# Optimization experiments

Measured on AMD Instinct MI355X. Metric: run time of the kernel, lower is better.

The kernel has to match this reference:

```python
import jax, jax.numpy as jnp
import numpy as np

N = 8192
F_IN = 128
F_OUT = 64
ALPHA = 0.2
NEG_INF = -9.0e15  # matches -9000000000000000.0 in the torch source


def setup_inputs() -> dict:
    key = jax.random.key(0)
    k1, k2, k3, k4 = jax.random.split(key, 4)
    h = jax.random.normal(k1, (N, F_IN), dtype=jnp.float32)
    adj = jax.random.randint(k2, (N, N), 0, 2).astype(jnp.int32)
    W = jax.random.normal(k3, (F_IN, F_OUT), dtype=jnp.float32) * 0.05
    a = jax.random.normal(k4, (2 * F_OUT,), dtype=jnp.float32) * 0.05
    return {"h": h, "adj": adj, "W": W, "a": a}


def reference(h, adj, W, a):
    # Wh: [N, F_OUT]
    Wh = h @ W
    # a([Wh_i ; Wh_j]) == Wh_i @ a1 + Wh_j @ a2 -> avoid O(N^2*2F) concat
    a1, a2 = a[:F_OUT], a[F_OUT:]
    s_src = Wh @ a1  # [N] contribution of row node i
    s_dst = Wh @ a2  # [N] contribution of col node j
    e = jax.nn.leaky_relu(s_src[:, None] + s_dst[None, :], negative_slope=ALPHA)  # [N, N]
    e = jnp.where(adj > 0, e, NEG_INF)
    attention = jax.nn.softmax(e, axis=1)  # [N, N]
    h_prime = attention @ Wh  # [N, F_OUT]
    return jax.nn.elu(h_prime)
```

## Files before the change

kernel.cpp:

```cpp
#include <hip/hip_runtime.h>
#include <hip/hip_bf16.h>

#define N 8192
#define FIN 128
#define FOUT 64
#define CSPLIT 4
#define CHUNK (N / CSPLIT)
#define M 32
#define TILE 64
#define NT (CHUNK / TILE)
#define LOG2E 1.44269504f

typedef __attribute__((ext_vector_type(4))) float f32x4;
typedef __attribute__((ext_vector_type(4))) int i32x4;
typedef __attribute__((ext_vector_type(8))) short bf16x8;

#define GLOAD_LDS16(gp, lp)                                                    \
    __builtin_amdgcn_global_load_lds(                                          \
        (const __attribute__((address_space(1))) void*)(gp),                   \
        (__attribute__((address_space(3))) void*)(lp), 16, 0, 0)

__global__ __launch_bounds__(256) void wh_kernel(
    const float* __restrict__ h, const float* __restrict__ W,
    const float* __restrict__ a,
    __hip_bfloat16* __restrict__ whT, float* __restrict__ s_src,
    float* __restrict__ s_dst) {
    __shared__ float Wl[FIN * FOUT];
    const int w = threadIdx.x >> 6;
    const int lane = threadIdx.x & 63;
#pragma unroll
    for (int q = 0; q < 8; ++q) {
        const int i = w * 8 + q;
        GLOAD_LDS16(W + i * 256 + lane * 4, &Wl[i * 256]);
    }
    asm volatile("s_waitcnt vmcnt(0)" ::: "memory");
    __syncthreads();

    const int row = blockIdx.x * 4 + w;
    const float* hr = h + (size_t)row * FIN;
    float acc = 0.f;
#pragma unroll
    for (int k0 = 0; k0 < FIN; k0 += 4) {
        f32x4 hv = *(const f32x4*)(hr + k0);
        acc += hv[0] * Wl[(k0 + 0) * FOUT + lane];
        acc += hv[1] * Wl[(k0 + 1) * FOUT + lane];
        acc += hv[2] * Wl[(k0 + 2) * FOUT + lane];
        acc += hv[3] * Wl[(k0 + 3) * FOUT + lane];
    }
    whT[(size_t)lane * N + row] = __float2bfloat16(acc);
    float s1 = acc * a[lane];
    float s2 = acc * a[FOUT + lane];
#pragma unroll
    for (int mm = 32; mm >= 1; mm >>= 1) {
        s1 += __shfl_xor(s1, mm, 64);
        s2 += __shfl_xor(s2, mm, 64);
    }
    if (lane == 0) { s_src[row] = s1 * LOG2E; s_dst[row] = s2 * LOG2E; }
}

__global__ __launch_bounds__(256, 4) void gat_partial(
    const int* __restrict__ adj, const __hip_bfloat16* __restrict__ whT,
    const float* __restrict__ s_src, const float* __restrict__ s_dst,
    float* __restrict__ numP, float* __restrict__ denP) {
    union SMem {
        struct {
            int adjb[2][M][TILE];
            short whb[2][FOUT][TILE];
            float sdl[CHUNK];
        } s;
        struct { float pC[2][M][FOUT]; float pD[2][M]; } e;
    };
    __shared__ SMem sm;

    const int tid = threadIdx.x;
    const int w = tid >> 6, lane = tid & 63;
    const int m = lane & 15, kg = lane >> 4;
    const int wr = w >> 1, wc = w & 1;
    const int rg = blockIdx.x >> 2;
    const int c = blockIdx.x & 3;
    const int ibase = rg * M;
    const int cb = c * CHUNK;
    const int aRow = wr * 16 + m;
    const float ssrc = s_src[ibase + aRow];
    const int sidx = w * 2;

    f32x4 acc[4] = {{0,0,0,0},{0,0,0,0},{0,0,0,0},{0,0,0,0}};
    f32x4 acc4 = {0,0,0,0};
    const short oneb = (m == 0) ? (short)0x3F80 : (short)0;
    const bf16x8 bones = {oneb, oneb, oneb, oneb, oneb, oneb, oneb, oneb};

    auto stage = [&](int t, int buf) {
        const int gcol = cb + t * TILE;
#pragma unroll
        for (int q = 0; q < 2; ++q) {
            const int idx = sidx + q;
            const int r = idx * 4 + (lane >> 4);
            const int b = ((lane & 15) * 16) ^ ((r & 15) << 4);
            GLOAD_LDS16(adj + (size_t)(ibase + r) * N + gcol + (b >> 2),
                        &sm.s.adjb[buf][idx * 4][0]);
        }
#pragma unroll
        for (int q = 0; q < 2; ++q) {
            const int idx = sidx + q;
            const int f = idx * 8 + (lane >> 3);
            const int b = ((lane & 7) * 16) ^ ((f & 7) << 4);
            GLOAD_LDS16(whT + (size_t)f * N + gcol + (b >> 1),
                        &sm.s.whb[buf][idx * 8][0]);
        }
    };

#pragma unroll
    for (int q = 0; q < 2; ++q) {
        const int i = sidx + q;
        GLOAD_LDS16(s_dst + cb + i * 256 + lane * 4, &sm.s.sdl[i * 256]);
    }
    stage(0, 0);
    asm volatile("s_waitcnt vmcnt(0)" ::: "memory");
    __builtin_amdgcn_s_barrier();

    for (int t = 0; t < NT; ++t) {
        const int buf = t & 1;
        if (t + 1 < NT) stage(t + 1, buf ^ 1);

        {
            const int kcol = wc * 32 + kg * 8;
            const char* adjbase = (const char*)&sm.s.adjb[buf][0][0];
            const int aswz = (aRow & 15) << 4;
            i32x4 a0 = *(const i32x4*)(adjbase + aRow * 256 + ((kcol * 4) ^ aswz));
            i32x4 a1 = *(const i32x4*)(adjbase + aRow * 256 + ((kcol * 4 + 16) ^ aswz));
            f32x4 d0 = *(const f32x4*)&sm.s.sdl[t * TILE + kcol];
            f32x4 d1 = *(const f32x4*)&sm.s.sdl[t * TILE + kcol + 4];
            const char* whbase = (const char*)&sm.s.whb[buf][0][0];
            const int wswz = (m & 7) << 4;
            bf16x8 bq0 = *(const bf16x8*)(whbase + (0 * 16 + m) * 128 + ((kcol * 2) ^ wswz));
            bf16x8 bq1 = *(const bf16x8*)(whbase + (1 * 16 + m) * 128 + ((kcol * 2) ^ wswz));
            bf16x8 bq2 = *(const bf16x8*)(whbase + (2 * 16 + m) * 128 + ((kcol * 2) ^ wswz));
            bf16x8 bq3 = *(const bf16x8*)(whbase + (3 * 16 + m) * 128 + ((kcol * 2) ^ wswz));

            float p[8];
#pragma unroll
            for (int e = 0; e < 4; ++e) {
                float x = ssrc + d0[e];
                float xl = fmaxf(x, 0.2f * x);
                float pe;
                asm("v_exp_f32 %0, %1" : "=v"(pe) : "v"(xl));
                p[e] = (a0[e] != 0) ? pe : 0.f;
            }
#pragma unroll
            for (int e = 0; e < 4; ++e) {
                float x = ssrc + d1[e];
                float xl = fmaxf(x, 0.2f * x);
                float pe;
                asm("v_exp_f32 %0, %1" : "=v"(pe) : "v"(xl));
                p[4 + e] = (a1[e] != 0) ? pe : 0.f;
            }
            union { bf16x8 v; unsigned u[4]; } afr;
#pragma unroll
            for (int q = 0; q < 4; ++q) {
                asm("v_cvt_pk_bf16_f32 %0, %1, %2"
                    : "=v"(afr.u[q]) : "v"(p[2 * q]), "v"(p[2 * q + 1]));
            }

            acc[0] = __builtin_amdgcn_mfma_f32_16x16x32_bf16(afr.v, bq0, acc[0], 0, 0, 0);
            acc[1] = __builtin_amdgcn_mfma_f32_16x16x32_bf16(afr.v, bq1, acc[1], 0, 0, 0);
            acc[2] = __builtin_amdgcn_mfma_f32_16x16x32_bf16(afr.v, bq2, acc[2], 0, 0, 0);
            acc[3] = __builtin_amdgcn_mfma_f32_16x16x32_bf16(afr.v, bq3, acc[3], 0, 0, 0);
            acc4   = __builtin_amdgcn_mfma_f32_16x16x32_bf16(afr.v, bones, acc4, 0, 0, 0);
        }

        asm volatile("s_waitcnt vmcnt(0)" ::: "memory");
        __builtin_amdgcn_s_barrier();
    }

#pragma unroll
    for (int r = 0; r < 4; ++r) {
#pragma unroll
        for (int q = 0; q < 4; ++q) {
            sm.e.pC[wc][wr * 16 + kg * 4 + r][q * 16 + m] = acc[q][r];
        }
    }
    if (m == 0) {
#pragma unroll
        for (int r = 0; r < 4; ++r) {
            sm.e.pD[wc][wr * 16 + kg * 4 + r] = acc4[r];
        }
    }
    __syncthreads();

    float* numC = numP + (size_t)c * N * FOUT;
    float* denC = denP + (size_t)c * N;
#pragma unroll
    for (int k = 0; k < 8; ++k) {
        int idx = k * 256 + tid;
        int i = idx >> 6, f = idx & 63;
        float num = sm.e.pC[0][i][f] + sm.e.pC[1][i][f];
        numC[(size_t)(ibase + i) * FOUT + f] = num;
        if (f == 0) {
            denC[ibase + i] = sm.e.pD[0][i] + sm.e.pD[1][i];
        }
    }
}

__global__ __launch_bounds__(256) void gat_combine(
    const float* __restrict__ numP, const float* __restrict__ denP,
    float* __restrict__ out) {
    int idx = blockIdx.x * 256 + threadIdx.x;
    int row = idx >> 6;
    float num = 0.f, den = 0.f;
#pragma unroll
    for (int cc = 0; cc < CSPLIT; ++cc) {
        num += numP[(size_t)cc * N * FOUT + idx];
        den += denP[(size_t)cc * N + row];
    }
    float v = num / den;
    out[idx] = (v > 0.f) ? v : expm1f(v);
}

extern "C" void kernel_launch(void* const* d_in, const int* in_sizes, int n_in,
                              void* d_out, int out_size, void* d_ws, size_t ws_size,
                              hipStream_t stream) {
    const float* h = (const float*)d_in[0];
    const int* adj = (const int*)d_in[1];
    const float* W = (const float*)d_in[2];
    const float* a = (const float*)d_in[3];
    float* out = (float*)d_out;

    char* ws = (char*)d_ws;
    __hip_bfloat16* whT = (__hip_bfloat16*)ws;
    float* s_src = (float*)(ws + (size_t)FOUT * N * sizeof(__hip_bfloat16));
    float* s_dst = s_src + N;
    float* numP = s_dst + N;
    float* denP = numP + (size_t)CSPLIT * N * FOUT;

    hipLaunchKernelGGL(wh_kernel, dim3(N / 4), dim3(256), 0, stream,
                       h, W, a, whT, s_src, s_dst);
    hipLaunchKernelGGL(gat_partial, dim3((N / M) * CSPLIT), dim3(256), 0, stream,
                       adj, whT, s_src, s_dst, numP, denP);
    hipLaunchKernelGGL(gat_combine, dim3(N * FOUT / 256), dim3(256), 0, stream,
                       numP, denP, out);
}
```

Measured before the change: 74.98 us.

## Triple-buffer staging, halve row tile, split features across waves, double column split

Moves the attention-partial kernel from 32 to 16 rows per block and from 4 to 8 column chunks. Waves now split the feature dimension instead of the row dimension, and the ones-vector denominator MFMA is issued by only half the waves. Staging becomes a three-deep LDS ring with partial vmcnt waits, so two tiles are kept in flight and global-load latency is hidden. The cost is that adj reuse of each whT tile drops, whT traffic doubles, and there are more partial sums for the combine kernel to read.

```diff
diff --git a/kernel.cpp b/kernel.cpp
--- a/kernel.cpp
+++ b/kernel.cpp
@@ -4,9 +4,9 @@
 #define N 8192
 #define FIN 128
 #define FOUT 64
-#define CSPLIT 4
+#define CSPLIT 8
 #define CHUNK (N / CSPLIT)
-#define M 32
+#define M 16
 #define TILE 64
 #define NT (CHUNK / TILE)
 #define LOG2E 1.44269504f
@@ -64,8 +64,8 @@
     float* __restrict__ numP, float* __restrict__ denP) {
     union SMem {
         struct {
-            int adjb[2][M][TILE];
-            short whb[2][FOUT][TILE];
+            int adjb[3][M][TILE];
+            short whb[3][FOUT][TILE];
             float sdl[CHUNK];
         } s;
         struct { float pC[2][M][FOUT]; float pD[2][M]; } e;
@@ -75,33 +75,31 @@
     const int tid = threadIdx.x;
     const int w = tid >> 6, lane = tid & 63;
     const int m = lane & 15, kg = lane >> 4;
-    const int wr = w >> 1, wc = w & 1;
-    const int rg = blockIdx.x >> 2;
-    const int c = blockIdx.x & 3;
+    const int wk = w & 1, wf = w >> 1;
+    const int rg = blockIdx.x >> 3;
+    const int c = blockIdx.x & 7;
     const int ibase = rg * M;
     const int cb = c * CHUNK;
-    const int aRow = wr * 16 + m;
-    const float ssrc = s_src[ibase + aRow];
-    const int sidx = w * 2;
-
-    f32x4 acc[4] = {{0,0,0,0},{0,0,0,0},{0,0,0,0},{0,0,0,0}};
+    const float ssrc = s_src[ibase + m];
+    const int kcol = wk * 32 + kg * 8;
+
+    f32x4 acc[2] = {{0,0,0,0},{0,0,0,0}};
     f32x4 acc4 = {0,0,0,0};
     const short oneb = (m == 0) ? (short)0x3F80 : (short)0;
     const bf16x8 bones = {oneb, oneb, oneb, oneb, oneb, oneb, oneb, oneb};
 
-    auto stage = [&](int t, int buf) {
+    auto stage = [&](int t) {
+        const int buf = t % 3;
         const int gcol = cb + t * TILE;
-#pragma unroll
-        for (int q = 0; q < 2; ++q) {
-            const int idx = sidx + q;
-            const int r = idx * 4 + (lane >> 4);
+        {
+            const int r = w * 4 + (lane >> 4);
             const int b = ((lane & 15) * 16) ^ ((r & 15) << 4);
             GLOAD_LDS16(adj + (size_t)(ibase + r) * N + gcol + (b >> 2),
-                        &sm.s.adjb[buf][idx * 4][0]);
+                        &sm.s.adjb[buf][w * 4][0]);
         }
 #pragma unroll
         for (int q = 0; q < 2; ++q) {
-            const int idx = sidx + q;
+            const int idx = w * 2 + q;
             const int f = idx * 8 + (lane >> 3);
             const int b = ((lane & 7) * 16) ^ ((f & 7) << 4);
             GLOAD_LDS16(whT + (size_t)f * N + gcol + (b >> 1),
@@ -109,33 +107,27 @@
         }
     };
 
-#pragma unroll
-    for (int q = 0; q < 2; ++q) {
-        const int i = sidx + q;
-        GLOAD_LDS16(s_dst + cb + i * 256 + lane * 4, &sm.s.sdl[i * 256]);
-    }
-    stage(0, 0);
-    asm volatile("s_waitcnt vmcnt(0)" ::: "memory");
+    GLOAD_LDS16(s_dst + cb + w * 256 + lane * 4, &sm.s.sdl[w * 256]);
+    stage(0);
+    stage(1);
+    asm volatile("s_waitcnt vmcnt(3)" ::: "memory");
     __builtin_amdgcn_s_barrier();
 
     for (int t = 0; t < NT; ++t) {
-        const int buf = t & 1;
-        if (t + 1 < NT) stage(t + 1, buf ^ 1);
+        if (t + 2 < NT) stage(t + 2);
 
         {
-            const int kcol = wc * 32 + kg * 8;
+            const int buf = t % 3;
             const char* adjbase = (const char*)&sm.s.adjb[buf][0][0];
-            const int aswz = (aRow & 15) << 4;
-            i32x4 a0 = *(const i32x4*)(adjbase + aRow * 256 + ((kcol * 4) ^ aswz));
-            i32x4 a1 = *(const i32x4*)(adjbase + aRow * 256 + ((kcol * 4 + 16) ^ aswz));
+            const int aswz = m << 4;
+            i32x4 a0 = *(const i32x4*)(adjbase + m * 256 + ((kcol * 4) ^ aswz));
+            i32x4 a1 = *(const i32x4*)(adjbase + m * 256 + ((kcol * 4 + 16) ^ aswz));
             f32x4 d0 = *(const f32x4*)&sm.s.sdl[t * TILE + kcol];
             f32x4 d1 = *(const f32x4*)&sm.s.sdl[t * TILE + kcol + 4];
             const char* whbase = (const char*)&sm.s.whb[buf][0][0];
             const int wswz = (m & 7) << 4;
-            bf16x8 bq0 = *(const bf16x8*)(whbase + (0 * 16 + m) * 128 + ((kcol * 2) ^ wswz));
-            bf16x8 bq1 = *(const bf16x8*)(whbase + (1 * 16 + m) * 128 + ((kcol * 2) ^ wswz));
-            bf16x8 bq2 = *(const bf16x8*)(whbase + (2 * 16 + m) * 128 + ((kcol * 2) ^ wswz));
-            bf16x8 bq3 = *(const bf16x8*)(whbase + (3 * 16 + m) * 128 + ((kcol * 2) ^ wswz));
+            bf16x8 bq0 = *(const bf16x8*)(whbase + (wf * 32 + 0 * 16 + m) * 128 + ((kcol * 2) ^ wswz));
+            bf16x8 bq1 = *(const bf16x8*)(whbase + (wf * 32 + 1 * 16 + m) * 128 + ((kcol * 2) ^ wswz));
 
             float p[8];
 #pragma unroll
@@ -163,26 +155,30 @@
 
             acc[0] = __builtin_amdgcn_mfma_f32_16x16x32_bf16(afr.v, bq0, acc[0], 0, 0, 0);
             acc[1] = __builtin_amdgcn_mfma_f32_16x16x32_bf16(afr.v, bq1, acc[1], 0, 0, 0);
-            acc[2] = __builtin_amdgcn_mfma_f32_16x16x32_bf16(afr.v, bq2, acc[2], 0, 0, 0);
-            acc[3] = __builtin_amdgcn_mfma_f32_16x16x32_bf16(afr.v, bq3, acc[3], 0, 0, 0);
-            acc4   = __builtin_amdgcn_mfma_f32_16x16x32_bf16(afr.v, bones, acc4, 0, 0, 0);
-        }
-
-        asm volatile("s_waitcnt vmcnt(0)" ::: "memory");
+            if (wf == 0) {
+                acc4 = __builtin_amdgcn_mfma_f32_16x16x32_bf16(afr.v, bones, acc4, 0, 0, 0);
+            }
+        }
+
+        if (t + 2 < NT) {
+            asm volatile("s_waitcnt vmcnt(3)" ::: "memory");
+        } else {
+            asm volatile("s_waitcnt vmcnt(0)" ::: "memory");
+        }
         __builtin_amdgcn_s_barrier();
     }
 
 #pragma unroll
     for (int r = 0; r < 4; ++r) {
 #pragma unroll
-        for (int q = 0; q < 4; ++q) {
-            sm.e.pC[wc][wr * 16 + kg * 4 + r][q * 16 + m] = acc[q][r];
-        }
-    }
-    if (m == 0) {
+        for (int q = 0; q < 2; ++q) {
+            sm.e.pC[wk][kg * 4 + r][wf * 32 + q * 16 + m] = acc[q][r];
+        }
+    }
+    if (wf == 0 && m == 0) {
 #pragma unroll
         for (int r = 0; r < 4; ++r) {
-            sm.e.pD[wc][wr * 16 + kg * 4 + r] = acc4[r];
+            sm.e.pD[wk][kg * 4 + r] = acc4[r];
         }
     }
     __syncthreads();
@@ -190,7 +186,7 @@
     float* numC = numP + (size_t)c * N * FOUT;
     float* denC = denP + (size_t)c * N;
 #pragma unroll
-    for (int k = 0; k < 8; ++k) {
+    for (int k = 0; k < 4; ++k) {
         int idx = k * 256 + tid;
         int i = idx >> 6, f = idx & 63;
         float num = sm.e.pC[0][i][f] + sm.e.pC[1][i][f];
@@ -229,8 +225,8 @@
     __hip_bfloat16* whT = (__hip_bfloat16*)ws;
     float* s_src = (float*)(ws + (size_t)FOUT * N * sizeof(__hip_bfloat16));
     float* s_dst = s_src + N;
-    float* numP = s_dst + N;
-    float* denP = numP + (size_t)CSPLIT * N * FOUT;
+    float* denP = s_dst + N;
+    float* numP = denP + (size_t)CSPLIT * N;
 
     hipLaunchKernelGGL(wh_kernel, dim3(N / 4), dim3(256), 0, stream,
                        h, W, a, whT, s_src, s_dst);
```

Result: slower. 105.3 us (+40.4%).

## Fuse split-K combine into partial kernel via last-block atomic counter

Applied to the files above, without the earlier changes.

Removes the separate combine kernel. Each row group now has an atomic counter, and the last of the four column-split blocks to finish reads all partials and writes the ELU output. The counters are zeroed inside wh_kernel. wh_kernel also now computes four rows per wave, so each W value loaded from shared memory is reused four times and the grid shrinks. This saves one kernel launch and a pass over the output, at the cost of threadfences, an atomic per block and a serialized tail on the last block.

```diff
diff --git a/kernel.cpp b/kernel.cpp
--- a/kernel.cpp
+++ b/kernel.cpp
@@ -24,10 +24,11 @@
     const float* __restrict__ h, const float* __restrict__ W,
     const float* __restrict__ a,
     __hip_bfloat16* __restrict__ whT, float* __restrict__ s_src,
-    float* __restrict__ s_dst) {
+    float* __restrict__ s_dst, int* __restrict__ cnt) {
     __shared__ float Wl[FIN * FOUT];
     const int w = threadIdx.x >> 6;
     const int lane = threadIdx.x & 63;
+    if (threadIdx.x == 0 && blockIdx.x < (N / M)) cnt[blockIdx.x] = 0;
 #pragma unroll
     for (int q = 0; q < 8; ++q) {
         const int i = w * 8 + q;
@@ -36,32 +37,39 @@
     asm volatile("s_waitcnt vmcnt(0)" ::: "memory");
     __syncthreads();
 
-    const int row = blockIdx.x * 4 + w;
-    const float* hr = h + (size_t)row * FIN;
-    float acc = 0.f;
-#pragma unroll
+    const int rbase = blockIdx.x * 16 + w * 4;
+    float acc[4] = {0.f, 0.f, 0.f, 0.f};
     for (int k0 = 0; k0 < FIN; k0 += 4) {
-        f32x4 hv = *(const f32x4*)(hr + k0);
-        acc += hv[0] * Wl[(k0 + 0) * FOUT + lane];
-        acc += hv[1] * Wl[(k0 + 1) * FOUT + lane];
-        acc += hv[2] * Wl[(k0 + 2) * FOUT + lane];
-        acc += hv[3] * Wl[(k0 + 3) * FOUT + lane];
-    }
-    whT[(size_t)lane * N + row] = __float2bfloat16(acc);
-    float s1 = acc * a[lane];
-    float s2 = acc * a[FOUT + lane];
-#pragma unroll
-    for (int mm = 32; mm >= 1; mm >>= 1) {
-        s1 += __shfl_xor(s1, mm, 64);
-        s2 += __shfl_xor(s2, mm, 64);
-    }
-    if (lane == 0) { s_src[row] = s1 * LOG2E; s_dst[row] = s2 * LOG2E; }
+        float wv0 = Wl[(k0 + 0) * FOUT + lane];
+        float wv1 = Wl[(k0 + 1) * FOUT + lane];
+        float wv2 = Wl[(k0 + 2) * FOUT + lane];
+        float wv3 = Wl[(k0 + 3) * FOUT + lane];
+#pragma unroll
+        for (int rr = 0; rr < 4; ++rr) {
+            f32x4 hv = *(const f32x4*)(h + (size_t)(rbase + rr) * FIN + k0);
+            acc[rr] += hv[0] * wv0 + hv[1] * wv1 + hv[2] * wv2 + hv[3] * wv3;
+        }
+    }
+#pragma unroll
+    for (int rr = 0; rr < 4; ++rr) {
+        const int row = rbase + rr;
+        whT[(size_t)lane * N + row] = __float2bfloat16(acc[rr]);
+        float s1 = acc[rr] * a[lane];
+        float s2 = acc[rr] * a[FOUT + lane];
+#pragma unroll
+        for (int mm = 32; mm >= 1; mm >>= 1) {
+            s1 += __shfl_xor(s1, mm, 64);
+            s2 += __shfl_xor(s2, mm, 64);
+        }
+        if (lane == 0) { s_src[row] = s1 * LOG2E; s_dst[row] = s2 * LOG2E; }
+    }
 }
 
 __global__ __launch_bounds__(256, 4) void gat_partial(
     const int* __restrict__ adj, const __hip_bfloat16* __restrict__ whT,
     const float* __restrict__ s_src, const float* __restrict__ s_dst,
-    float* __restrict__ numP, float* __restrict__ denP) {
+    float* __restrict__ numP, float* __restrict__ denP,
+    int* __restrict__ cnt, float* __restrict__ out) {
     union SMem {
         struct {
             int adjb[2][M][TILE];
@@ -199,21 +207,31 @@
             denC[ibase + i] = sm.e.pD[0][i] + sm.e.pD[1][i];
         }
     }
-}
-
-__global__ __launch_bounds__(256) void gat_combine(
-    const float* __restrict__ numP, const float* __restrict__ denP,
-    float* __restrict__ out) {
-    int idx = blockIdx.x * 256 + threadIdx.x;
-    int row = idx >> 6;
-    float num = 0.f, den = 0.f;
-#pragma unroll
-    for (int cc = 0; cc < CSPLIT; ++cc) {
-        num += numP[(size_t)cc * N * FOUT + idx];
-        den += denP[(size_t)cc * N + row];
-    }
-    float v = num / den;
-    out[idx] = (v > 0.f) ? v : expm1f(v);
+
+    __threadfence();
+    __syncthreads();
+    int* flagp = (int*)&sm;
+    if (tid == 0) {
+        int old = atomicAdd(&cnt[rg], 1);
+        *flagp = (old == CSPLIT - 1) ? 1 : 0;
+    }
+    __syncthreads();
+    if (*flagp) {
+        __threadfence();
+#pragma unroll
+        for (int k = 0; k < 8; ++k) {
+            int idx = k * 256 + tid;
+            int i = idx >> 6, f = idx & 63;
+            float num = 0.f, den = 0.f;
+#pragma unroll
+            for (int cc = 0; cc < CSPLIT; ++cc) {
+                num += numP[(size_t)cc * N * FOUT + (size_t)(ibase + i) * FOUT + f];
+                den += denP[(size_t)cc * N + ibase + i];
+            }
+            float v = num / den;
+            out[(size_t)(ibase + i) * FOUT + f] = (v > 0.f) ? v : expm1f(v);
+        }
+    }
 }
 
 extern "C" void kernel_launch(void* const* d_in, const int* in_sizes, int n_in,
@@ -231,11 +249,10 @@
     float* s_dst = s_src + N;
     float* numP = s_dst + N;
     float* denP = numP + (size_t)CSPLIT * N * FOUT;
-
-    hipLaunchKernelGGL(wh_kernel, dim3(N / 4), dim3(256), 0, stream,
-                       h, W, a, whT, s_src, s_dst);
+    int* cnt = (int*)(denP + (size_t)CSPLIT * N);
+
+    hipLaunchKernelGGL(wh_kernel, dim3(N / 16), dim3(256), 0, stream,
+                       h, W, a, whT, s_src, s_dst, cnt);
     hipLaunchKernelGGL(gat_partial, dim3((N / M) * CSPLIT), dim3(256), 0, stream,
-                       adj, whT, s_src, s_dst, numP, denP);
-    hipLaunchKernelGGL(gat_combine, dim3(N * FOUT / 256), dim3(256), 0, stream,
-                       numP, denP, out);
+                       adj, whT, s_src, s_dst, numP, denP, cnt, out);
 }
```

Measured after the change: 264.5 us. 3.53x slower.
